# Kernel optimization log

Measured on AMD Instinct MI355X. Metric: run time of the kernel, lower is better.

The kernel has to match this reference:

```python
import jax, jax.numpy as jnp
import numpy as np

N, D, H, E = 50000, 128, 128, 800000


def setup_inputs() -> dict:
    key = jax.random.key(0)
    ks = jax.random.split(key, 12)
    p = lambda k, shape: jax.random.normal(k, shape, dtype=jnp.float32) * 0.02
    z = lambda n: jnp.zeros((n,), jnp.float32)
    return {
        "x1": jax.random.normal(ks[0], (N, D), dtype=jnp.float32),
        "edge_index1": jax.random.randint(ks[1], (2, E), 0, N, dtype=jnp.int32),
        "x2": jax.random.normal(ks[2], (N, D), dtype=jnp.float32),
        "edge_index2": jax.random.randint(ks[3], (2, E), 0, N, dtype=jnp.int32),
        "enc_w1": p(ks[4], (D, H)), "enc_b1": z(H),
        "enc_w2": p(ks[5], (H, H)), "enc_b2": z(H),
        "conv1_w": p(ks[6], (H, H)), "conv1_b": z(H),
        "conv2_w": p(ks[7], (H, H)), "conv2_b": z(H),
        "sim_w1": p(ks[8], (4 * H, H)), "sim_b1": z(H),
        "sim_w2": p(ks[9], (H, 1)), "sim_b2": z(1),
    }


def reference(x1, edge_index1, x2, edge_index2,
              enc_w1, enc_b1, enc_w2, enc_b2,
              conv1_w, conv1_b, conv2_w, conv2_b,
              sim_w1, sim_b1, sim_w2, sim_b2):
    def gcn(x, ei, W, b):
        row, col = ei[0], ei[1]            # [E], [E]
        h = x @ W + b                      # [N, H]
        n = x.shape[0]
        deg = jax.ops.segment_sum(jnp.ones(row.shape[0], h.dtype), row, num_segments=n)
        dis = jnp.where(deg > 0, deg ** -0.5, 0.0)   # deg^-0.5, inf -> 0
        norm = dis[row] * dis[col]         # [E]
        msg = h[col] * norm[:, None]       # gather + per-edge scale, [E, H]
        return jax.ops.segment_sum(msg, row, num_segments=n)  # scatter-add

    def embed(x, ei):
        h = jax.nn.relu(x @ enc_w1 + enc_b1) @ enc_w2 + enc_b2  # encoder MLP
        h = jax.nn.relu(gcn(h, ei, conv1_w, conv1_b))
        h = jax.nn.relu(gcn(h, ei, conv2_w, conv2_b))
        return h.mean(axis=0)              # mean pooling -> [H]

    g1 = embed(x1, edge_index1)
    g2 = embed(x2, edge_index2)
    c = jnp.concatenate([g1, g2, jnp.abs(g1 - g2), g1 * g2], axis=-1)  # [4H]
    return jax.nn.relu(c @ sim_w1 + sim_b1) @ sim_w2 + sim_b2          # [1]
```

## Files before the change

kernel.cpp:

```cpp
#include <hip/hip_runtime.h>

#define HD 128

typedef _Float16 f16x8 __attribute__((ext_vector_type(8)));
typedef _Float16 f16x2 __attribute__((ext_vector_type(2)));
typedef float f32x4 __attribute__((ext_vector_type(4)));

__global__ void k_deg_slot(const int* __restrict__ ei0, const int* __restrict__ ei1,
                           int E, int N, int* __restrict__ deg2,
                           unsigned short* __restrict__ slot) {
  int g = blockIdx.y;
  const int* rows = g ? ei1 : ei0;
  int* deg = deg2 + g * N;
  unsigned short* sl = slot + (size_t)g * E;
  int base = (blockIdx.x * 256 + threadIdx.x) * 4;
  if (base + 3 < E) {
    int4 r = *(const int4*)(rows + base);
    union { unsigned short us[4]; uint2 v; } s;
    s.us[0] = (unsigned short)atomicAdd(&deg[r.x], 1);
    s.us[1] = (unsigned short)atomicAdd(&deg[r.y], 1);
    s.us[2] = (unsigned short)atomicAdd(&deg[r.z], 1);
    s.us[3] = (unsigned short)atomicAdd(&deg[r.w], 1);
    *(uint2*)(sl + base) = s.v;
  } else {
    for (int e = base; e < E; ++e)
      sl[e] = (unsigned short)atomicAdd(&deg[rows[e]], 1);
  }
}

__global__ void k_csr_fill(const int* __restrict__ ei0, const int* __restrict__ ei1,
                           int E, int N, const int* __restrict__ offs,
                           const unsigned short* __restrict__ slot,
                           unsigned short* __restrict__ csr_col) {
  int g = blockIdx.y;
  const int* eg = (g ? ei1 : ei0);
  const int* ob = offs + g * N;
  const unsigned short* sl = slot + (size_t)g * E;
  int base = (blockIdx.x * 256 + threadIdx.x) * 4;
  if (base + 3 < E) {
    int4 r = *(const int4*)(eg + base);
    int4 c = *(const int4*)(eg + E + base);
    uint2 sv = *(const uint2*)(sl + base);
    csr_col[ob[r.x] + (sv.x & 0xffff)] = (unsigned short)c.x;
    csr_col[ob[r.y] + (sv.x >> 16)]    = (unsigned short)c.y;
    csr_col[ob[r.z] + (sv.y & 0xffff)] = (unsigned short)c.z;
    csr_col[ob[r.w] + (sv.y >> 16)]    = (unsigned short)c.w;
  } else {
    for (int e = base; e < E; ++e)
      csr_col[ob[eg[e]] + sl[e]] = (unsigned short)eg[E + e];
  }
}

template<bool RELU, bool SCALE, bool CVT>
__device__ __forceinline__ void gemm_block(
    _Float16* lds, int bi,
    const _Float16* __restrict__ Ab, const float* __restrict__ Af0,
    const float* __restrict__ Af1, const float* __restrict__ Wg,
    const float* __restrict__ bias, const float* __restrict__ scale,
    _Float16* __restrict__ C, int N, int Ntot) {
  const int tid = threadIdx.x;
  #pragma unroll
  for (int i = 0; i < 16; ++i) {
    int flat = i * 1024 + tid * 4;
    int k = flat >> 7, n0 = flat & 127;
    float4 w4 = *(const float4*)(Wg + flat);
    int kc = k >> 5, q = (k >> 3) & 3, j = k & 7;
    float wv[4] = {w4.x, w4.y, w4.z, w4.w};
    #pragma unroll
    for (int d = 0; d < 4; ++d) {
      int n = n0 + d;
      lds[(size_t)(((n >> 4) * 4 + kc) * 64 + 16 * q + (n & 15)) * 8 + j] = (_Float16)wv[d];
    }
  }
  __syncthreads();

  const int lane = tid & 63;
  const int wave = tid >> 6;
  const int n16 = lane & 15, q = lane >> 4;
  const int rowbase = bi * 256 + wave * 64;

  int arow[4];
  #pragma unroll
  for (int t = 0; t < 4; ++t) {
    int r = rowbase + 16 * t + n16;
    arow[t] = (r < Ntot) ? r : (Ntot - 1);
  }

  f32x4 acc[4][8];
  #pragma unroll
  for (int t = 0; t < 4; ++t)
    #pragma unroll
    for (int nt = 0; nt < 8; ++nt) acc[t][nt] = (f32x4){0.f, 0.f, 0.f, 0.f};

  #pragma unroll
  for (int kc = 0; kc < 4; ++kc) {
    f16x8 a[4];
    #pragma unroll
    for (int t = 0; t < 4; ++t) {
      if (CVT) {
        int r = arow[t];
        const float* src = (r < N) ? (Af0 + (size_t)r * HD) : (Af1 + (size_t)(r - N) * HD);
        float4 u0 = *(const float4*)(src + kc * 32 + q * 8);
        float4 u1 = *(const float4*)(src + kc * 32 + q * 8 + 4);
        union { _Float16 h[8]; f16x8 v; } tmp;
        tmp.h[0] = (_Float16)u0.x; tmp.h[1] = (_Float16)u0.y;
        tmp.h[2] = (_Float16)u0.z; tmp.h[3] = (_Float16)u0.w;
        tmp.h[4] = (_Float16)u1.x; tmp.h[5] = (_Float16)u1.y;
        tmp.h[6] = (_Float16)u1.z; tmp.h[7] = (_Float16)u1.w;
        a[t] = tmp.v;
      } else {
        a[t] = *(const f16x8*)(Ab + (size_t)arow[t] * HD + kc * 32 + q * 8);
      }
    }
    #pragma unroll
    for (int nt = 0; nt < 8; ++nt) {
      f16x8 b = *(const f16x8*)&lds[(size_t)((nt * 4 + kc) * 64 + lane) * 8];
      #pragma unroll
      for (int t = 0; t < 4; ++t)
        acc[t][nt] = __builtin_amdgcn_mfma_f32_16x16x32_f16(a[t], b, acc[t][nt], 0, 0, 0);
    }
  }

  float bv[8];
  #pragma unroll
  for (int nt = 0; nt < 8; ++nt) bv[nt] = bias[nt * 16 + n16];

  #pragma unroll
  for (int t = 0; t < 4; ++t) {
    #pragma unroll
    for (int r = 0; r < 4; ++r) {
      int row = rowbase + 16 * t + 4 * q + r;
      if (row < Ntot) {
        float s = SCALE ? scale[row] : 1.0f;
        #pragma unroll
        for (int nt = 0; nt < 8; ++nt) {
          float v = acc[t][nt][r] + bv[nt];
          if (RELU) v = fmaxf(v, 0.f);
          if (SCALE) v *= s;
          C[(size_t)row * HD + nt * 16 + n16] = (_Float16)v;
        }
      }
    }
  }
}

template<bool RELU, bool SCALE, bool CVT, int AUX>
__global__ __launch_bounds__(256, 2) void k_gemm_aux(
    const _Float16* __restrict__ Ab, const float* __restrict__ Af0,
    const float* __restrict__ Af1, const float* __restrict__ Wg,
    const float* __restrict__ bias, const float* __restrict__ scale,
    _Float16* __restrict__ C, int N, int Ntot, int gemmBlocks,
    const int* __restrict__ deg, int* __restrict__ offs,
    int* __restrict__ partials, float* __restrict__ dis,
    int scanBlocks, int Etot) {
  __shared__ _Float16 lds[16384];
  int bi = blockIdx.x;
  if (bi < gemmBlocks) {
    gemm_block<RELU, SCALE, CVT>(lds, bi, Ab, Af0, Af1, Wg, bias, scale, C, N, Ntot);
    return;
  }
  int b = bi - gemmBlocks;
  int t = threadIdx.x;
  if (AUX == 1) {
    int* s = (int*)lds;
    int i = b * 256 + t;
    int v = (i < Ntot) ? deg[i] : 0;
    s[t] = v;
    __syncthreads();
    #pragma unroll
    for (int off = 1; off < 256; off <<= 1) {
      int x = (t >= off) ? s[t - off] : 0;
      __syncthreads();
      s[t] += x;
      __syncthreads();
    }
    if (i < Ntot) {
      offs[i] = s[t] - v;
      dis[i] = (v > 0) ? (1.0f / sqrtf((float)v)) : 0.0f;
    }
    if (t == 255) partials[b] = s[255];
  } else if (AUX == 2) {
    int* s = (int*)lds;
    int P = scanBlocks;
    int v0 = (t < P) ? partials[t] : 0;
    int v1 = (t + 256 < P) ? partials[t + 256] : 0;
    s[t] = v0;
    s[t + 256] = v1;
    __syncthreads();
    #pragma unroll
    for (int off = 1; off < 256; off <<= 1) {
      int x0 = (t >= off) ? s[t - off] : 0;
      int x1 = (t >= off) ? s[256 + t - off] : 0;
      __syncthreads();
      s[t] += x0;
      s[256 + t] += x1;
      __syncthreads();
    }
    int tot0 = s[255];
    if (t < P) partials[t] = s[t] - v0;
    if (t + 256 < P) partials[t + 256] = s[256 + t] + tot0 - v1;
  } else if (AUX == 3) {
    int i = b * 256 + t;
    if (i < Ntot) offs[i] += partials[b];
    if (b == 0 && t == 0) offs[Ntot] = Etot;
  }
}

template<bool POOL>
__global__ __launch_bounds__(256) void k_aggregate(
    const _Float16* __restrict__ T, const int* __restrict__ offs,
    const unsigned short* __restrict__ csr_col, const float* __restrict__ dis,
    _Float16* __restrict__ out, float* __restrict__ poolrep, int N, int Ntot) {
  __shared__ float red[4][128];
  const int lane = threadIdx.x & 63;
  const int wave = threadIdx.x >> 6;
  const int gw = blockIdx.x * 4 + wave;
  const int sub = lane >> 4, c16 = lane & 15;

  f16x2 hacc[4];
  #pragma unroll
  for (int j = 0; j < 4; ++j) hacc[j] = (f16x2){(_Float16)0.f, (_Float16)0.f};

  if (gw < Ntot) {
    const int beg = offs[gw], end = offs[gw + 1];
    const uint4* Tg = (const uint4*)(T + (size_t)(gw >= N ? N : 0) * HD);
    for (int e = beg; e < end; e += 16) {
      uint4 v[4];
      #pragma unroll
      for (int gp = 0; gp < 4; ++gp) {
        v[gp] = make_uint4(0, 0, 0, 0);
        if (e + 4 * gp < end) {
          int eg = e + 4 * gp + sub;
          bool valid = (eg < end);
          int ce = valid ? eg : (end - 1);
          int col = csr_col[ce];
          uint4 t = Tg[(size_t)col * 16 + c16];
          if (valid) v[gp] = t;
        }
      }
      #pragma unroll
      for (int gp = 0; gp < 4; ++gp) {
        union { uint4 u; f16x2 h[4]; } w;
        w.u = v[gp];
        hacc[0] += w.h[0];
        hacc[1] += w.h[1];
        hacc[2] += w.h[2];
        hacc[3] += w.h[3];
      }
    }
  }

  float ax[8];
  #pragma unroll
  for (int j = 0; j < 4; ++j) {
    ax[2 * j]     = (float)hacc[j][0];
    ax[2 * j + 1] = (float)hacc[j][1];
  }
  #pragma unroll
  for (int j = 0; j < 8; ++j) {
    ax[j] += __shfl_xor(ax[j], 32, 64);
    ax[j] += __shfl_xor(ax[j], 16, 64);
  }
  float dr = (gw < Ntot) ? dis[gw] : 0.f;
  #pragma unroll
  for (int j = 0; j < 8; ++j) ax[j] = fmaxf(ax[j] * dr, 0.f);

  if (!POOL) {
    if (gw < Ntot && sub == 0) {
      union { uint4 u; _Float16 h[8]; } o;
      #pragma unroll
      for (int j = 0; j < 8; ++j) o.h[j] = (_Float16)ax[j];
      ((uint4*)out)[(size_t)gw * 16 + c16] = o.u;
    }
  } else {
    if (sub == 0) {
      *(float4*)&red[wave][c16 * 8]     = make_float4(ax[0], ax[1], ax[2], ax[3]);
      *(float4*)&red[wave][c16 * 8 + 4] = make_float4(ax[4], ax[5], ax[6], ax[7]);
    }
    __syncthreads();
    int t = threadIdx.x;
    if (t < 128) {
      float s = red[0][t] + red[1][t] + red[2][t] + red[3][t];
      int g = (blockIdx.x * 4 >= N) ? 1 : 0;
      atomicAdd(&poolrep[(size_t)((blockIdx.x & 15) * 2 + g) * 128 + t], s);
    }
  }
}

__global__ void k_final(const float* __restrict__ poolrep,
                        const float* __restrict__ W1, const float* __restrict__ b1,
                        const float* __restrict__ W2, const float* __restrict__ b2,
                        float* __restrict__ out, float invN) {
  __shared__ float cs[512];
  __shared__ float red[2];
  int t = threadIdx.x;
  float g1 = 0.f, g2 = 0.f;
  #pragma unroll
  for (int r = 0; r < 16; ++r) {
    g1 += poolrep[r * 256 + t];
    g2 += poolrep[r * 256 + 128 + t];
  }
  g1 *= invN;
  g2 *= invN;
  cs[t] = g1;
  cs[128 + t] = g2;
  cs[256 + t] = fabsf(g1 - g2);
  cs[384 + t] = g1 * g2;
  __syncthreads();
  float acc = b1[t];
  #pragma unroll 8
  for (int i = 0; i < 512; ++i) acc = fmaf(cs[i], W1[(size_t)i * HD + t], acc);
  float h = fmaxf(acc, 0.f);
  float v = h * W2[t];
  #pragma unroll
  for (int off = 32; off > 0; off >>= 1) v += __shfl_down(v, off, 64);
  if ((t & 63) == 0) red[t >> 6] = v;
  __syncthreads();
  if (t == 0) out[0] = red[0] + red[1] + b2[0];
}

extern "C" void kernel_launch(void* const* d_in, const int* in_sizes, int n_in,
                              void* d_out, int out_size, void* d_ws, size_t ws_size,
                              hipStream_t stream) {
  const float* x1     = (const float*)d_in[0];
  const int*   ei1    = (const int*)d_in[1];
  const float* x2     = (const float*)d_in[2];
  const int*   ei2    = (const int*)d_in[3];
  const float* W_in[4] = {(const float*)d_in[4], (const float*)d_in[6],
                          (const float*)d_in[8], (const float*)d_in[10]};
  const float* B_in[4] = {(const float*)d_in[5], (const float*)d_in[7],
                          (const float*)d_in[9], (const float*)d_in[11]};
  const float* sim_w1 = (const float*)d_in[12];
  const float* sim_b1 = (const float*)d_in[13];
  const float* sim_w2 = (const float*)d_in[14];
  const float* sim_b2 = (const float*)d_in[15];

  const int N = in_sizes[0] / HD;
  const int E = in_sizes[1] / 2;
  const int Ntot = 2 * N;

  _Float16* sp = (_Float16*)d_ws;
  _Float16* bufA = sp; sp += (size_t)Ntot * HD;
  _Float16* bufB = sp; sp += (size_t)Ntot * HD;
  float* fp = (float*)sp;
  float* dis     = fp; fp += Ntot;
  float* poolrep = fp; fp += 16 * 256;
  int* ip = (int*)fp;
  int* deg2     = ip; ip += Ntot;
  int* offs     = ip; ip += Ntot + 1;
  int* partials = ip; ip += 512;
  ip = (int*)(((uintptr_t)ip + 15) & ~(uintptr_t)15);
  unsigned short* slot = (unsigned short*)ip;
  unsigned short* csr_col = slot + 2 * (size_t)E;

  const int gemmBlocks = (Ntot + 255) / 256;
  const int scanBlocks = (Ntot + 255) / 256;
  const int aggBlocks  = (Ntot + 3) / 4;
  const dim3 edgeGrid(((E + 3) / 4 + 255) / 256, 2);

  hipMemsetAsync(poolrep, 0, (16 * 256 + Ntot) * sizeof(float), stream);

  k_deg_slot<<<edgeGrid, 256, 0, stream>>>(ei1, ei2, E, N, deg2, slot);

  k_gemm_aux<true, false, true, 1><<<gemmBlocks + scanBlocks, 256, 0, stream>>>(
      nullptr, x1, x2, W_in[0], B_in[0], nullptr, bufA, N, Ntot, gemmBlocks,
      deg2, offs, partials, dis, scanBlocks, 2 * E);

  k_gemm_aux<false, false, false, 2><<<gemmBlocks + 1, 256, 0, stream>>>(
      bufA, nullptr, nullptr, W_in[1], B_in[1], nullptr, bufB, N, Ntot, gemmBlocks,
      deg2, offs, partials, dis, scanBlocks, 2 * E);

  k_gemm_aux<false, true, false, 3><<<gemmBlocks + scanBlocks, 256, 0, stream>>>(
      bufB, nullptr, nullptr, W_in[2], B_in[2], dis, bufA, N, Ntot, gemmBlocks,
      deg2, offs, partials, dis, scanBlocks, 2 * E);

  k_csr_fill<<<edgeGrid, 256, 0, stream>>>(ei1, ei2, E, N, offs, slot, csr_col);

  k_aggregate<false><<<aggBlocks, 256, 0, stream>>>(bufA, offs, csr_col, dis, bufB, nullptr, N, Ntot);

  k_gemm_aux<false, true, false, 0><<<gemmBlocks, 256, 0, stream>>>(
      bufB, nullptr, nullptr, W_in[3], B_in[3], dis, bufA, N, Ntot, gemmBlocks,
      deg2, offs, partials, dis, scanBlocks, 2 * E);

  k_aggregate<true><<<aggBlocks, 256, 0, stream>>>(bufA, offs, csr_col, dis, nullptr, poolrep, N, Ntot);

  k_final<<<1, 128, 0, stream>>>(poolrep, sim_w1, sim_b1, sim_w2, sim_b2,
                                 (float*)d_out, 1.0f / (float)N);
}
```

Before: 429.5 us.

## Fuse degree counting into first GEMM, pre-swizzle weights, drop offset-fix pass

The separate degree/slot kernel is folded into the auxiliary blocks of the first GEMM launch, which also pre-converts the three later weight matrices into an fp16 swizzled LDS layout so later GEMMs copy them directly. The third scan pass that added block partials into offsets is removed; csr_fill and aggregate add the partials on the fly. GEMM tiles shrink from 256 to 128 rows with occupancy hint raised to 4 blocks. This trims kernel launches and per-block weight conversion, at the cost of extra partials lookups in the gather-heavy kernels.

```diff
diff --git a/kernel.cpp b/kernel.cpp
--- a/kernel.cpp
+++ b/kernel.cpp
@@ -6,70 +6,33 @@
 typedef _Float16 f16x2 __attribute__((ext_vector_type(2)));
 typedef float f32x4 __attribute__((ext_vector_type(4)));
 
-__global__ void k_deg_slot(const int* __restrict__ ei0, const int* __restrict__ ei1,
-                           int E, int N, int* __restrict__ deg2,
-                           unsigned short* __restrict__ slot) {
-  int g = blockIdx.y;
-  const int* rows = g ? ei1 : ei0;
-  int* deg = deg2 + g * N;
-  unsigned short* sl = slot + (size_t)g * E;
-  int base = (blockIdx.x * 256 + threadIdx.x) * 4;
-  if (base + 3 < E) {
-    int4 r = *(const int4*)(rows + base);
-    union { unsigned short us[4]; uint2 v; } s;
-    s.us[0] = (unsigned short)atomicAdd(&deg[r.x], 1);
-    s.us[1] = (unsigned short)atomicAdd(&deg[r.y], 1);
-    s.us[2] = (unsigned short)atomicAdd(&deg[r.z], 1);
-    s.us[3] = (unsigned short)atomicAdd(&deg[r.w], 1);
-    *(uint2*)(sl + base) = s.v;
-  } else {
-    for (int e = base; e < E; ++e)
-      sl[e] = (unsigned short)atomicAdd(&deg[rows[e]], 1);
-  }
-}
-
-__global__ void k_csr_fill(const int* __restrict__ ei0, const int* __restrict__ ei1,
-                           int E, int N, const int* __restrict__ offs,
-                           const unsigned short* __restrict__ slot,
-                           unsigned short* __restrict__ csr_col) {
-  int g = blockIdx.y;
-  const int* eg = (g ? ei1 : ei0);
-  const int* ob = offs + g * N;
-  const unsigned short* sl = slot + (size_t)g * E;
-  int base = (blockIdx.x * 256 + threadIdx.x) * 4;
-  if (base + 3 < E) {
-    int4 r = *(const int4*)(eg + base);
-    int4 c = *(const int4*)(eg + E + base);
-    uint2 sv = *(const uint2*)(sl + base);
-    csr_col[ob[r.x] + (sv.x & 0xffff)] = (unsigned short)c.x;
-    csr_col[ob[r.y] + (sv.x >> 16)]    = (unsigned short)c.y;
-    csr_col[ob[r.z] + (sv.y & 0xffff)] = (unsigned short)c.z;
-    csr_col[ob[r.w] + (sv.y >> 16)]    = (unsigned short)c.w;
-  } else {
-    for (int e = base; e < E; ++e)
-      csr_col[ob[eg[e]] + sl[e]] = (unsigned short)eg[E + e];
-  }
-}
-
-template<bool RELU, bool SCALE, bool CVT>
+template<bool RELU, bool SCALE, bool CVT, bool WF16>
 __device__ __forceinline__ void gemm_block(
     _Float16* lds, int bi,
     const _Float16* __restrict__ Ab, const float* __restrict__ Af0,
-    const float* __restrict__ Af1, const float* __restrict__ Wg,
+    const float* __restrict__ Af1, const void* __restrict__ Wsrc,
     const float* __restrict__ bias, const float* __restrict__ scale,
     _Float16* __restrict__ C, int N, int Ntot) {
   const int tid = threadIdx.x;
-  #pragma unroll
-  for (int i = 0; i < 16; ++i) {
-    int flat = i * 1024 + tid * 4;
-    int k = flat >> 7, n0 = flat & 127;
-    float4 w4 = *(const float4*)(Wg + flat);
-    int kc = k >> 5, q = (k >> 3) & 3, j = k & 7;
-    float wv[4] = {w4.x, w4.y, w4.z, w4.w};
-    #pragma unroll
-    for (int d = 0; d < 4; ++d) {
-      int n = n0 + d;
-      lds[(size_t)(((n >> 4) * 4 + kc) * 64 + 16 * q + (n & 15)) * 8 + j] = (_Float16)wv[d];
+  if (WF16) {
+    const _Float16* Wf = (const _Float16*)Wsrc;
+    #pragma unroll
+    for (int i = 0; i < 8; ++i)
+      *(float4*)&lds[tid * 8 + i * 2048] = *(const float4*)&Wf[tid * 8 + i * 2048];
+  } else {
+    const float* Wg = (const float*)Wsrc;
+    #pragma unroll
+    for (int i = 0; i < 16; ++i) {
+      int flat = i * 1024 + tid * 4;
+      int k = flat >> 7, n0 = flat & 127;
+      float4 w4 = *(const float4*)(Wg + flat);
+      int kc = k >> 5, q = (k >> 3) & 3, j = k & 7;
+      float wv[4] = {w4.x, w4.y, w4.z, w4.w};
+      #pragma unroll
+      for (int d = 0; d < 4; ++d) {
+        int n = n0 + d;
+        lds[(size_t)(((n >> 4) * 4 + kc) * 64 + 16 * q + (n & 15)) * 8 + j] = (_Float16)wv[d];
+      }
     }
   }
   __syncthreads();
@@ -77,26 +40,26 @@
   const int lane = tid & 63;
   const int wave = tid >> 6;
   const int n16 = lane & 15, q = lane >> 4;
-  const int rowbase = bi * 256 + wave * 64;
-
-  int arow[4];
-  #pragma unroll
-  for (int t = 0; t < 4; ++t) {
+  const int rowbase = bi * 128 + wave * 32;
+
+  int arow[2];
+  #pragma unroll
+  for (int t = 0; t < 2; ++t) {
     int r = rowbase + 16 * t + n16;
     arow[t] = (r < Ntot) ? r : (Ntot - 1);
   }
 
-  f32x4 acc[4][8];
-  #pragma unroll
-  for (int t = 0; t < 4; ++t)
+  f32x4 acc[2][8];
+  #pragma unroll
+  for (int t = 0; t < 2; ++t)
     #pragma unroll
     for (int nt = 0; nt < 8; ++nt) acc[t][nt] = (f32x4){0.f, 0.f, 0.f, 0.f};
 
   #pragma unroll
   for (int kc = 0; kc < 4; ++kc) {
-    f16x8 a[4];
-    #pragma unroll
-    for (int t = 0; t < 4; ++t) {
+    f16x8 a[2];
+    #pragma unroll
+    for (int t = 0; t < 2; ++t) {
       if (CVT) {
         int r = arow[t];
         const float* src = (r < N) ? (Af0 + (size_t)r * HD) : (Af1 + (size_t)(r - N) * HD);
@@ -116,7 +79,7 @@
     for (int nt = 0; nt < 8; ++nt) {
       f16x8 b = *(const f16x8*)&lds[(size_t)((nt * 4 + kc) * 64 + lane) * 8];
       #pragma unroll
-      for (int t = 0; t < 4; ++t)
+      for (int t = 0; t < 2; ++t)
         acc[t][nt] = __builtin_amdgcn_mfma_f32_16x16x32_f16(a[t], b, acc[t][nt], 0, 0, 0);
     }
   }
@@ -126,7 +89,7 @@
   for (int nt = 0; nt < 8; ++nt) bv[nt] = bias[nt * 16 + n16];
 
   #pragma unroll
-  for (int t = 0; t < 4; ++t) {
+  for (int t = 0; t < 2; ++t) {
     #pragma unroll
     for (int r = 0; r < 4; ++r) {
       int row = rowbase + 16 * t + 4 * q + r;
@@ -144,27 +107,67 @@
   }
 }
 
-template<bool RELU, bool SCALE, bool CVT, int AUX>
-__global__ __launch_bounds__(256, 2) void k_gemm_aux(
+template<bool RELU, bool SCALE, bool CVT, bool WF16, int AUX>
+__global__ __launch_bounds__(256, 4) void k_fused(
     const _Float16* __restrict__ Ab, const float* __restrict__ Af0,
-    const float* __restrict__ Af1, const float* __restrict__ Wg,
+    const float* __restrict__ Af1, const void* __restrict__ Wsrc,
     const float* __restrict__ bias, const float* __restrict__ scale,
-    _Float16* __restrict__ C, int N, int Ntot, int gemmBlocks,
-    const int* __restrict__ deg, int* __restrict__ offs,
-    int* __restrict__ partials, float* __restrict__ dis,
-    int scanBlocks, int Etot) {
+    _Float16* __restrict__ C, int N, int Ntot, int auxN,
+    const int* __restrict__ ei0, const int* __restrict__ ei1, int E,
+    int* __restrict__ deg2, unsigned short* __restrict__ slot,
+    const float* __restrict__ w1, const float* __restrict__ w2,
+    const float* __restrict__ w3, _Float16* __restrict__ WfOut, int degB,
+    int* __restrict__ offs, int* __restrict__ partials,
+    float* __restrict__ dis, int scanBlocks) {
   __shared__ _Float16 lds[16384];
-  int bi = blockIdx.x;
-  if (bi < gemmBlocks) {
-    gemm_block<RELU, SCALE, CVT>(lds, bi, Ab, Af0, Af1, Wg, bias, scale, C, N, Ntot);
+  const int bi = blockIdx.x;
+  const int t = threadIdx.x;
+  if (bi >= auxN) {
+    gemm_block<RELU, SCALE, CVT, WF16>(lds, bi - auxN, Ab, Af0, Af1, Wsrc,
+                                       bias, scale, C, N, Ntot);
     return;
   }
-  int b = bi - gemmBlocks;
-  int t = threadIdx.x;
   if (AUX == 1) {
+    if (bi < 2 * degB) {
+      int g = (bi >= degB);
+      int cb = bi - g * degB;
+      const int* rows = g ? ei1 : ei0;
+      int* deg = deg2 + g * N;
+      unsigned short* sl = slot + (size_t)g * E;
+      int base = (cb * 256 + t) * 4;
+      if (base + 3 < E) {
+        int4 r = *(const int4*)(rows + base);
+        union { unsigned short us[4]; uint2 v; } s;
+        s.us[0] = (unsigned short)atomicAdd(&deg[r.x], 1);
+        s.us[1] = (unsigned short)atomicAdd(&deg[r.y], 1);
+        s.us[2] = (unsigned short)atomicAdd(&deg[r.z], 1);
+        s.us[3] = (unsigned short)atomicAdd(&deg[r.w], 1);
+        *(uint2*)(sl + base) = s.v;
+      } else {
+        for (int e = base; e < E; ++e)
+          sl[e] = (unsigned short)atomicAdd(&deg[rows[e]], 1);
+      }
+    } else {
+      int wb = bi - 2 * degB;
+      int m = wb >> 3;
+      const float* Wg = (m == 0) ? w1 : (m == 1) ? w2 : w3;
+      int idx0 = (wb & 7) * 2048 + t * 8;
+      float4 u0 = *(const float4*)(Wg + idx0);
+      float4 u1 = *(const float4*)(Wg + idx0 + 4);
+      int k = idx0 >> 7, n0 = idx0 & 127;
+      int kc = k >> 5, q2 = (k >> 3) & 3, j = k & 7;
+      _Float16* dst = WfOut + (size_t)m * 16384;
+      float vv[8] = {u0.x, u0.y, u0.z, u0.w, u1.x, u1.y, u1.z, u1.w};
+      #pragma unroll
+      for (int d = 0; d < 8; ++d) {
+        int n = n0 + d;
+        dst[(size_t)(((n >> 4) * 4 + kc) * 64 + 16 * q2 + (n & 15)) * 8 + j] = (_Float16)vv[d];
+      }
+    }
+  } else if (AUX == 2) {
     int* s = (int*)lds;
-    int i = b * 256 + t;
-    int v = (i < Ntot) ? deg[i] : 0;
+    int i = bi * 256 + t;
+    int v = (i < Ntot) ? deg2[i] : 0;
     s[t] = v;
     __syncthreads();
     #pragma unroll
@@ -178,8 +181,8 @@
       offs[i] = s[t] - v;
       dis[i] = (v > 0) ? (1.0f / sqrtf((float)v)) : 0.0f;
     }
-    if (t == 255) partials[b] = s[255];
-  } else if (AUX == 2) {
+    if (t == 255) partials[bi] = s[255];
+  } else if (AUX == 3) {
     int* s = (int*)lds;
     int P = scanBlocks;
     int v0 = (t < P) ? partials[t] : 0;
@@ -199,18 +202,41 @@
     int tot0 = s[255];
     if (t < P) partials[t] = s[t] - v0;
     if (t + 256 < P) partials[t + 256] = s[256 + t] + tot0 - v1;
-  } else if (AUX == 3) {
-    int i = b * 256 + t;
-    if (i < Ntot) offs[i] += partials[b];
-    if (b == 0 && t == 0) offs[Ntot] = Etot;
+  }
+}
+
+__global__ void k_csr_fill(const int* __restrict__ ei0, const int* __restrict__ ei1,
+                           int E, int N, const int* __restrict__ offs,
+                           const int* __restrict__ partials,
+                           const unsigned short* __restrict__ slot,
+                           unsigned short* __restrict__ csr_col) {
+  int g = blockIdx.y;
+  const int* eg = (g ? ei1 : ei0);
+  const int* ob = offs + g * N;
+  const int* pb = partials;
+  const unsigned short* sl = slot + (size_t)g * E;
+  int gN = g * N;
+  int base = (blockIdx.x * 256 + threadIdx.x) * 4;
+  if (base + 3 < E) {
+    int4 r = *(const int4*)(eg + base);
+    int4 c = *(const int4*)(eg + E + base);
+    uint2 sv = *(const uint2*)(sl + base);
+    csr_col[ob[r.x] + pb[(gN + r.x) >> 8] + (sv.x & 0xffff)] = (unsigned short)c.x;
+    csr_col[ob[r.y] + pb[(gN + r.y) >> 8] + (sv.x >> 16)]    = (unsigned short)c.y;
+    csr_col[ob[r.z] + pb[(gN + r.z) >> 8] + (sv.y & 0xffff)] = (unsigned short)c.z;
+    csr_col[ob[r.w] + pb[(gN + r.w) >> 8] + (sv.y >> 16)]    = (unsigned short)c.w;
+  } else {
+    for (int e = base; e < E; ++e)
+      csr_col[ob[eg[e]] + pb[(gN + eg[e]) >> 8] + sl[e]] = (unsigned short)eg[E + e];
   }
 }
 
 template<bool POOL>
 __global__ __launch_bounds__(256) void k_aggregate(
     const _Float16* __restrict__ T, const int* __restrict__ offs,
-    const unsigned short* __restrict__ csr_col, const float* __restrict__ dis,
-    _Float16* __restrict__ out, float* __restrict__ poolrep, int N, int Ntot) {
+    const int* __restrict__ partials, const unsigned short* __restrict__ csr_col,
+    const float* __restrict__ dis, _Float16* __restrict__ out,
+    float* __restrict__ poolrep, int N, int Ntot, int Etot) {
   __shared__ float red[4][128];
   const int lane = threadIdx.x & 63;
   const int wave = threadIdx.x >> 6;
@@ -222,7 +248,8 @@
   for (int j = 0; j < 4; ++j) hacc[j] = (f16x2){(_Float16)0.f, (_Float16)0.f};
 
   if (gw < Ntot) {
-    const int beg = offs[gw], end = offs[gw + 1];
+    const int beg = offs[gw] + partials[gw >> 8];
+    const int end = (gw + 1 == Ntot) ? Etot : (offs[gw + 1] + partials[(gw + 1) >> 8]);
     const uint4* Tg = (const uint4*)(T + (size_t)(gw >= N ? N : 0) * HD);
     for (int e = beg; e < end; e += 16) {
       uint4 v[4];
@@ -234,8 +261,8 @@
           bool valid = (eg < end);
           int ce = valid ? eg : (end - 1);
           int col = csr_col[ce];
-          uint4 t = Tg[(size_t)col * 16 + c16];
-          if (valid) v[gp] = t;
+          uint4 tv = Tg[(size_t)col * 16 + c16];
+          if (valid) v[gp] = tv;
         }
       }
       #pragma unroll
@@ -342,48 +369,50 @@
   _Float16* sp = (_Float16*)d_ws;
   _Float16* bufA = sp; sp += (size_t)Ntot * HD;
   _Float16* bufB = sp; sp += (size_t)Ntot * HD;
+  _Float16* WfB  = sp; sp += 3 * 16384;
   float* fp = (float*)sp;
   float* dis     = fp; fp += Ntot;
   float* poolrep = fp; fp += 16 * 256;
   int* ip = (int*)fp;
   int* deg2     = ip; ip += Ntot;
-  int* offs     = ip; ip += Ntot + 1;
+  int* offs     = ip; ip += Ntot;
   int* partials = ip; ip += 512;
   ip = (int*)(((uintptr_t)ip + 15) & ~(uintptr_t)15);
   unsigned short* slot = (unsigned short*)ip;
   unsigned short* csr_col = slot + 2 * (size_t)E;
 
-  const int gemmBlocks = (Ntot + 255) / 256;
-  const int scanBlocks = (Ntot + 255) / 256;
-  const int aggBlocks  = (Ntot + 3) / 4;
-  const dim3 edgeGrid(((E + 3) / 4 + 255) / 256, 2);
+  const int G = (Ntot + 127) / 128;
+  const int scanB = (Ntot + 255) / 256;
+  const int aggB  = (Ntot + 3) / 4;
+  const int degB  = (E + 1023) / 1024;
+  const dim3 fillGrid(((E + 3) / 4 + 255) / 256, 2);
 
   hipMemsetAsync(poolrep, 0, (16 * 256 + Ntot) * sizeof(float), stream);
 
-  k_deg_slot<<<edgeGrid, 256, 0, stream>>>(ei1, ei2, E, N, deg2, slot);
-
-  k_gemm_aux<true, false, true, 1><<<gemmBlocks + scanBlocks, 256, 0, stream>>>(
-      nullptr, x1, x2, W_in[0], B_in[0], nullptr, bufA, N, Ntot, gemmBlocks,
-      deg2, offs, partials, dis, scanBlocks, 2 * E);
-
-  k_gemm_aux<false, false, false, 2><<<gemmBlocks + 1, 256, 0, stream>>>(
-      bufA, nullptr, nullptr, W_in[1], B_in[1], nullptr, bufB, N, Ntot, gemmBlocks,
-      deg2, offs, partials, dis, scanBlocks, 2 * E);
-
-  k_gemm_aux<false, true, false, 3><<<gemmBlocks + scanBlocks, 256, 0, stream>>>(
-      bufB, nullptr, nullptr, W_in[2], B_in[2], dis, bufA, N, Ntot, gemmBlocks,
-      deg2, offs, partials, dis, scanBlocks, 2 * E);
-
-  k_csr_fill<<<edgeGrid, 256, 0, stream>>>(ei1, ei2, E, N, offs, slot, csr_col);
-
-  k_aggregate<false><<<aggBlocks, 256, 0, stream>>>(bufA, offs, csr_col, dis, bufB, nullptr, N, Ntot);
-
-  k_gemm_aux<false, true, false, 0><<<gemmBlocks, 256, 0, stream>>>(
-      bufB, nullptr, nullptr, W_in[3], B_in[3], dis, bufA, N, Ntot, gemmBlocks,
-      deg2, offs, partials, dis, scanBlocks, 2 * E);
-
-  k_aggregate<true><<<aggBlocks, 256, 0, stream>>>(bufA, offs, csr_col, dis, nullptr, poolrep, N, Ntot);
-
+  {
+    int auxN = 2 * degB + 24;
+    k_fused<true, false, true, false, 1><<<auxN + G, 256, 0, stream>>>(
+        nullptr, x1, x2, W_in[0], B_in[0], nullptr, bufA, N, Ntot, auxN,
+        ei1, ei2, E, deg2, slot, W_in[1], W_in[2], W_in[3], WfB, degB,
+        offs, partials, dis, scanB);
+  }
+  k_fused<false, false, false, true, 2><<<scanB + G, 256, 0, stream>>>(
+      bufA, nullptr, nullptr, WfB + 0 * 16384, B_in[1], nullptr, bufB, N, Ntot, scanB,
+      nullptr, nullptr, E, deg2, nullptr, nullptr, nullptr, nullptr, nullptr, degB,
+      offs, partials, dis, scanB);
+  k_fused<false, true, false, true, 3><<<1 + G, 256, 0, stream>>>(
+      bufB, nullptr, nullptr, WfB + 1 * 16384, B_in[2], dis, bufA, N, Ntot, 1,
+      nullptr, nullptr, E, deg2, nullptr, nullptr, nullptr, nullptr, nullptr, degB,
+      offs, partials, dis, scanB);
+  k_csr_fill<<<fillGrid, 256, 0, stream>>>(ei1, ei2, E, N, offs, partials, slot, csr_col);
+  k_aggregate<false><<<aggB, 256, 0, stream>>>(bufA, offs, partials, csr_col, dis,
+                                               bufB, nullptr, N, Ntot, 2 * E);
+  k_fused<false, true, false, true, 0><<<G, 256, 0, stream>>>(
+      bufB, nullptr, nullptr, WfB + 2 * 16384, B_in[3], dis, bufA, N, Ntot, 0,
+      nullptr, nullptr, E, deg2, nullptr, nullptr, nullptr, nullptr, nullptr, degB,
+      offs, partials, dis, scanB);
+  k_aggregate<true><<<aggB, 256, 0, stream>>>(bufA, offs, partials, csr_col, dis,
+                                              nullptr, poolrep, N, Ntot, 2 * E);
   k_final<<<1, 128, 0, stream>>>(poolrep, sim_w1, sim_b1, sim_w2, sim_b2,
                                  (float*)d_out, 1.0f / (float)N);
 }
```

After: 418.8 us. 2.5% less time.
